# Performance work log

Measured on AMD Instinct MI355X. Metric: run time of the kernel, lower is better.

## Reference

```python
import jax, jax.numpy as jnp
import numpy as np

N_NODES = 100000
N_GRAPHS = 512


def gcn_conv(x, W, b, src, dst, n):
    # PyG GCNConv: h = x @ W; add self-loops; sym-normalize; scatter-add to dst; + bias
    h = x @ W
    loop = jnp.arange(n, dtype=src.dtype)
    s = jnp.concatenate([src, loop])
    d = jnp.concatenate([dst, loop])
    deg = jax.ops.segment_sum(jnp.ones_like(d, dtype=h.dtype), d, num_segments=n)
    dinv = jnp.where(deg > 0, jax.lax.rsqrt(deg), 0.0)
    norm = dinv[s] * dinv[d]               # [E+N]
    msg = h[s] * norm[:, None]             # gather + scale
    out = jax.ops.segment_sum(msg, d, num_segments=n)
    return out + b


def setup_inputs() -> dict:
    key = jax.random.key(0)
    ks = jax.random.split(key, 12)
    F_in, H, C = 128, 128, 10
    x = jax.random.normal(ks[0], (N_NODES, F_in), dtype=jnp.float32)
    edge_index = jax.random.randint(ks[1], (2, 3200000), 0, N_NODES, dtype=jnp.int64)
    batch = jnp.sort(jax.random.randint(ks[2], (N_NODES,), 0, N_GRAPHS, dtype=jnp.int64))
    def glorot(k, fi, fo):
        s = jnp.sqrt(6.0 / (fi + fo))
        return jax.random.uniform(k, (fi, fo), dtype=jnp.float32, minval=-s, maxval=s)
    return {
        "x": x, "edge_index": edge_index, "batch": batch,
        "W_in": glorot(ks[3], F_in, H), "b_in": jnp.zeros((H,), jnp.float32),
        "W_h0": glorot(ks[4], H, H), "b_h0": jnp.zeros((H,), jnp.float32),
        "W_h1": glorot(ks[5], H, H), "b_h1": jnp.zeros((H,), jnp.float32),
        "W_out": glorot(ks[6], H, C), "b_out": jnp.zeros((C,), jnp.float32),
    }


def reference(x, edge_index, batch, W_in, b_in, W_h0, b_h0, W_h1, b_h1, W_out, b_out):
    src, dst = edge_index[0], edge_index[1]
    n = x.shape[0]
    h = jax.nn.relu(gcn_conv(x, W_in, b_in, src, dst, n))
    h = jax.nn.relu(gcn_conv(h, W_h0, b_h0, src, dst, n))
    h = jax.nn.relu(gcn_conv(h, W_h1, b_h1, src, dst, n))
    h = gcn_conv(h, W_out, b_out, src, dst, n)
    # global_mean_pool over graph ids
    sums = jax.ops.segment_sum(h, batch, num_segments=N_GRAPHS)
    cnts = jax.ops.segment_sum(jnp.ones((n,), h.dtype), batch, num_segments=N_GRAPHS)
    pooled = sums / jnp.maximum(cnts, 1.0)[:, None]
    return jax.nn.log_softmax(pooled, axis=-1)
```

## Files before the change

kernel.cpp:

```cpp
#include <hip/hip_runtime.h>
#include <math.h>

#define TPB 256
#define MAXDEG 80
#define SHIFT 8
#define BNODES 256
#define CAP 10240
#define EPB 4096
#define LSTR 136

typedef short bf16x8 __attribute__((ext_vector_type(8)));
typedef float f32x4 __attribute__((ext_vector_type(4)));

__device__ inline unsigned short f2bf(float f) {
    unsigned u = __float_as_uint(f);
    return (unsigned short)((u + 0x7fffu + ((u >> 16) & 1u)) >> 16);
}
__device__ inline float bflo(unsigned u) { return __uint_as_float(u << 16); }
__device__ inline float bfhi(unsigned u) { return __uint_as_float(u & 0xffff0000u); }



__global__ __launch_bounds__(TPB) void p1_k(const int* __restrict__ src,
                                            const int* __restrict__ dst,
                                            int* __restrict__ gbcnt,
                                            int* __restrict__ buckets, int E, int nb) {
    __shared__ int hist[512];
    __shared__ int lcur[512];
    int tid = threadIdx.x;
    for (int b = tid; b < nb; b += TPB) hist[b] = 0;
    __syncthreads();
    int e0 = blockIdx.x * EPB;
    int m = E - e0; if (m > EPB) m = EPB;
    for (int i = tid; i < m; i += TPB)
        atomicAdd(&hist[dst[e0 + i] >> SHIFT], 1);
    __syncthreads();
    for (int b = tid; b < nb; b += TPB) {
        int h = hist[b];
        lcur[b] = h ? atomicAdd(&gbcnt[b], h) : 0;
    }
    __syncthreads();
    for (int i = tid; i < m; i += TPB) {
        int d = dst[e0 + i];
        int s = src[e0 + i];
        int b = d >> SHIFT;
        int pos = atomicAdd(&lcur[b], 1);
        if (pos < CAP) buckets[(size_t)b * CAP + pos] = (s << SHIFT) | (d & (BNODES - 1));
    }
}


__global__ __launch_bounds__(TPB) void p2_k(const int* __restrict__ gbcnt,
                                            const int* __restrict__ buckets,
                                            int* __restrict__ csr,
                                            int* __restrict__ deg,
                                            float* __restrict__ dinv, int n, int nb,
                                            const float* __restrict__ W0,
                                            const float* __restrict__ W1,
                                            const float* __restrict__ W2,
                                            const float* __restrict__ W3,
                                            unsigned short* __restrict__ T0,
                                            unsigned short* __restrict__ T1,
                                            unsigned short* __restrict__ T2,
                                            unsigned short* __restrict__ T3,
                                            float* __restrict__ pool,
                                            int* __restrict__ cnt, int ng) {
    int b = blockIdx.x, tid = threadIdx.x;
    if (b >= nb) {
        int widx = b - nb;
        if (widx < 3) {
            const float* W = widx == 0 ? W0 : (widx == 1 ? W1 : W2);
            unsigned short* T = widx == 0 ? T0 : (widx == 1 ? T1 : T2);
            for (int idx = tid; idx < 16384; idx += TPB) {
                int nn = idx >> 7, kk = idx & 127;
                T[idx] = f2bf(W[kk * 128 + nn]);
            }
        } else {
            for (int idx = tid; idx < 2048; idx += TPB) {
                int nn = idx >> 7, kk = idx & 127;
                T3[idx] = nn < 10 ? f2bf(W3[kk * 10 + nn]) : (unsigned short)0;
            }
            for (int i = tid; i < ng * 10; i += TPB) pool[i] = 0.f;
            for (int i = tid; i < ng; i += TPB) cnt[i] = 0;
        }
        return;
    }
    __shared__ int lcnt[BNODES];
    lcnt[tid] = 0;
    __syncthreads();
    int m = gbcnt[b]; if (m > CAP) m = CAP;
    const int* bp = buckets + (size_t)b * CAP;
    int vb = b << SHIFT;
    for (int i = tid; i < m; i += TPB) {
        int rec = bp[i];
        int dl = rec & (BNODES - 1);
        int pos = atomicAdd(&lcnt[dl], 1);
        if (pos < MAXDEG) csr[(size_t)(vb + dl) * MAXDEG + pos] = rec >> SHIFT;
    }
    __syncthreads();
    int v = vb + tid;
    if (v < n) {
        int c = lcnt[tid];
        deg[v] = c < MAXDEG ? c : MAXDEG;
        dinv[v] = rsqrtf((float)(c + 1));
    }
}


__device__ __forceinline__ void mfma_tile(const unsigned short* Hs,
                                          const unsigned short* __restrict__ WT,
                                          const float* __restrict__ dinv,
                                          unsigned short* __restrict__ gout,
                                          int vb, int n, int w, int l) {
    f32x4 acc[2][8];
#pragma unroll
    for (int a = 0; a < 2; a++)
#pragma unroll
        for (int b = 0; b < 8; b++)
#pragma unroll
            for (int j = 0; j < 4; j++) acc[a][b][j] = 0.f;
    const int quad = l >> 4, lm = l & 15;
    const int mrow0 = w * 32;
#pragma unroll
    for (int ks = 0; ks < 4; ks++) {
        bf16x8 a0 = *(const bf16x8*)(Hs + (mrow0 + lm) * LSTR + ks * 32 + quad * 8);
        bf16x8 a1 = *(const bf16x8*)(Hs + (mrow0 + 16 + lm) * LSTR + ks * 32 + quad * 8);
#pragma unroll
        for (int nt = 0; nt < 8; nt++) {
            bf16x8 bf = *(const bf16x8*)(WT + (size_t)(nt * 16 + lm) * 128 + ks * 32 + quad * 8);
            acc[0][nt] = __builtin_amdgcn_mfma_f32_16x16x32_bf16(a0, bf, acc[0][nt], 0, 0, 0);
            acc[1][nt] = __builtin_amdgcn_mfma_f32_16x16x32_bf16(a1, bf, acc[1][nt], 0, 0, 0);
        }
    }
#pragma unroll
    for (int mt = 0; mt < 2; mt++) {
#pragma unroll
        for (int j = 0; j < 4; j++) {
            int r = vb + mrow0 + mt * 16 + quad * 4 + j;
            if (r < n) {
                float s = dinv[r];
#pragma unroll
                for (int nt = 0; nt < 8; nt++) {
                    size_t base = ((size_t)((nt >> 1) * n + r)) * 32;
                    gout[base + (nt & 1) * 16 + lm] = f2bf(acc[mt][nt][j] * s);
                }
            }
        }
    }
}


__global__ __launch_bounds__(256) void gemm_f32in(const float* __restrict__ x,
                                                  const unsigned short* __restrict__ WT,
                                                  const float* __restrict__ dinv,
                                                  unsigned short* __restrict__ gout, int n) {
    __shared__ unsigned short Hs[128 * LSTR];
    int tid = threadIdx.x;
    int vb = blockIdx.x * 128;
    for (int i = tid; i < 8192; i += 256) {
        int row = i >> 6, cw = i & 63;
        int gr = vb + row; if (gr > n - 1) gr = n - 1;
        float2 xv = *(const float2*)(x + (size_t)gr * 128 + cw * 2);
        unsigned pk = ((unsigned)f2bf(xv.y) << 16) | f2bf(xv.x);
        *(unsigned*)(Hs + row * LSTR + cw * 2) = pk;
    }
    __syncthreads();
    mfma_tile(Hs, WT, dinv, gout, vb, n, tid >> 6, tid & 63);
}


__global__ __launch_bounds__(256) void gemm_bf16in(const unsigned* __restrict__ hin,
                                                   const unsigned short* __restrict__ WT,
                                                   const float* __restrict__ dinv,
                                                   unsigned short* __restrict__ gout, int n) {
    __shared__ unsigned short Hs[128 * LSTR];
    int tid = threadIdx.x;
    int vb = blockIdx.x * 128;
    for (int i = tid; i < 8192; i += 256) {
        int row = i >> 6, cw = i & 63;
        int gr = vb + row; if (gr > n - 1) gr = n - 1;
        *(unsigned*)(Hs + row * LSTR + cw * 2) =
            hin[((size_t)((cw >> 4) * n + gr)) * 16 + (cw & 15)];
    }
    __syncthreads();
    mfma_tile(Hs, WT, dinv, gout, vb, n, tid >> 6, tid & 63);
}


__global__ __launch_bounds__(256) void thin_mfma(const unsigned* __restrict__ hin,
                                                 const unsigned short* __restrict__ WT3,
                                                 const float* __restrict__ dinv,
                                                 unsigned* __restrict__ g4u, int n) {
    __shared__ unsigned short Hs[128 * LSTR];
    int tid = threadIdx.x;
    int vb = blockIdx.x * 128;
    for (int i = tid; i < 8192; i += 256) {
        int row = i >> 6, cw = i & 63;
        int gr = vb + row; if (gr > n - 1) gr = n - 1;
        *(unsigned*)(Hs + row * LSTR + cw * 2) =
            hin[((size_t)((cw >> 4) * n + gr)) * 16 + (cw & 15)];
    }
    __syncthreads();
    int w = tid >> 6, l = tid & 63;
    int quad = l >> 4, lm = l & 15;
    int mrow0 = w * 32;
    f32x4 acc[2];
#pragma unroll
    for (int a = 0; a < 2; a++)
#pragma unroll
        for (int j = 0; j < 4; j++) acc[a][j] = 0.f;
#pragma unroll
    for (int ks = 0; ks < 4; ks++) {
        bf16x8 a0 = *(const bf16x8*)(Hs + (mrow0 + lm) * LSTR + ks * 32 + quad * 8);
        bf16x8 a1 = *(const bf16x8*)(Hs + (mrow0 + 16 + lm) * LSTR + ks * 32 + quad * 8);
        bf16x8 bf = *(const bf16x8*)(WT3 + (size_t)lm * 128 + ks * 32 + quad * 8);
        acc[0] = __builtin_amdgcn_mfma_f32_16x16x32_bf16(a0, bf, acc[0], 0, 0, 0);
        acc[1] = __builtin_amdgcn_mfma_f32_16x16x32_bf16(a1, bf, acc[1], 0, 0, 0);
    }
#pragma unroll
    for (int mt = 0; mt < 2; mt++) {
#pragma unroll
        for (int j = 0; j < 4; j++) {
            float self = acc[mt][j];
            float part = __shfl_down(self, 1, 64);
            int r = vb + mrow0 + mt * 16 + quad * 4 + j;
            if ((lm & 1) == 0 && lm < 10 && r < n) {
                float s = dinv[r];
                g4u[(size_t)r * 5 + (lm >> 1)] =
                    ((unsigned)f2bf(part * s) << 16) | f2bf(self * s);
            }
        }
    }
}


__global__ __launch_bounds__(256) void aggq_k(const unsigned* __restrict__ G,
                                              const float* __restrict__ dinv,
                                              const int* __restrict__ deg,
                                              const int* __restrict__ csr,
                                              const float* __restrict__ bias,
                                              unsigned* __restrict__ H, int n, int nblk) {
    int q = blockIdx.x / nblk;
    int blk = blockIdx.x - q * nblk;
    int w = threadIdx.x >> 6, l = threadIdx.x & 63;
    int sub = l >> 4, t = l & 15;
    int v = blk * 16 + w * 4 + sub;
    if (v >= n) return;
    const unsigned* Gq = G + (size_t)q * n * 16;
    unsigned u = Gq[(size_t)v * 16 + t];
    float a0 = bflo(u), a1 = bfhi(u);
    const int* cp = csr + (size_t)v * MAXDEG;
    int d = deg[v];
    int e = 0;
    for (; e + 8 <= d; e += 8) {
        int s0 = cp[e], s1 = cp[e + 1], s2 = cp[e + 2], s3 = cp[e + 3];
        int s4 = cp[e + 4], s5 = cp[e + 5], s6 = cp[e + 6], s7 = cp[e + 7];
        unsigned u0 = Gq[(size_t)s0 * 16 + t];
        unsigned u1 = Gq[(size_t)s1 * 16 + t];
        unsigned u2 = Gq[(size_t)s2 * 16 + t];
        unsigned u3 = Gq[(size_t)s3 * 16 + t];
        unsigned u4 = Gq[(size_t)s4 * 16 + t];
        unsigned u5 = Gq[(size_t)s5 * 16 + t];
        unsigned u6 = Gq[(size_t)s6 * 16 + t];
        unsigned u7 = Gq[(size_t)s7 * 16 + t];
        a0 += (bflo(u0) + bflo(u1)) + (bflo(u2) + bflo(u3))
            + (bflo(u4) + bflo(u5)) + (bflo(u6) + bflo(u7));
        a1 += (bfhi(u0) + bfhi(u1)) + (bfhi(u2) + bfhi(u3))
            + (bfhi(u4) + bfhi(u5)) + (bfhi(u6) + bfhi(u7));
    }
    for (; e < d; e++) {
        unsigned ux = Gq[(size_t)cp[e] * 16 + t];
        a0 += bflo(ux); a1 += bfhi(ux);
    }
    float2 bb = *(const float2*)(bias + q * 32 + 2 * t);
    float s = dinv[v];
    float o0 = fmaxf(s * a0 + bb.x, 0.f);
    float o1 = fmaxf(s * a1 + bb.y, 0.f);
    H[((size_t)q * n + v) * 16 + t] = ((unsigned)f2bf(o1) << 16) | f2bf(o0);
}


__global__ __launch_bounds__(TPB) void agg_thin_bf(const unsigned* __restrict__ g4u,
                                                   const float* __restrict__ dinv,
                                                   const int* __restrict__ deg,
                                                   const int* __restrict__ csr,
                                                   const float* __restrict__ bias,
                                                   float* __restrict__ out, int n) {
    int idx = blockIdx.x * TPB + threadIdx.x;
    if (idx >= n * 5) return;
    int v = idx / 5, t = idx - v * 5;
    unsigned u = g4u[(size_t)v * 5 + t];
    float acc0 = bflo(u), acc1 = bfhi(u);
    const int* cp = csr + (size_t)v * MAXDEG;
    int d = deg[v];
    int e = 0;
    for (; e + 4 <= d; e += 4) {
        unsigned u0 = g4u[(size_t)cp[e] * 5 + t];
        unsigned u1 = g4u[(size_t)cp[e + 1] * 5 + t];
        unsigned u2 = g4u[(size_t)cp[e + 2] * 5 + t];
        unsigned u3 = g4u[(size_t)cp[e + 3] * 5 + t];
        acc0 += (bflo(u0) + bflo(u1)) + (bflo(u2) + bflo(u3));
        acc1 += (bfhi(u0) + bfhi(u1)) + (bfhi(u2) + bfhi(u3));
    }
    for (; e < d; e++) {
        unsigned ux = g4u[(size_t)cp[e] * 5 + t];
        acc0 += bflo(ux); acc1 += bfhi(ux);
    }
    float s = dinv[v];
    out[(size_t)v * 10 + 2 * t]     = s * acc0 + bias[2 * t];
    out[(size_t)v * 10 + 2 * t + 1] = s * acc1 + bias[2 * t + 1];
}


#define POOL_SPAN 8

__global__ __launch_bounds__(TPB) void pool_k(const float* __restrict__ h,
                                              const int* __restrict__ batch,
                                              float* __restrict__ pool, int* __restrict__ cnt, int n) {
    __shared__ float lp[POOL_SPAN][10];
    __shared__ int lc[POOL_SPAN];
    __shared__ int g0;
    int tid = threadIdx.x;
    int v = blockIdx.x * TPB + tid;
    if (tid == 0) {
        int first = blockIdx.x * TPB;
        if (first > n - 1) first = n - 1;
        g0 = batch[first];
    }
    if (tid < POOL_SPAN) lc[tid] = 0;
    if (tid < POOL_SPAN * 10) lp[tid / 10][tid % 10] = 0.f;
    __syncthreads();
    if (v < n) {
        int gi = batch[v];
        int o = gi - g0;
        if (o < POOL_SPAN) {
            atomicAdd(&lc[o], 1);
#pragma unroll
            for (int c = 0; c < 10; c++) atomicAdd(&lp[o][c], h[(size_t)v * 10 + c]);
        } else {
            atomicAdd(&cnt[gi], 1);
#pragma unroll
            for (int c = 0; c < 10; c++) atomicAdd(&pool[gi * 10 + c], h[(size_t)v * 10 + c]);
        }
    }
    __syncthreads();
    if (tid < POOL_SPAN) {
        if (lc[tid] > 0) atomicAdd(&cnt[g0 + tid], lc[tid]);
    }
    if (tid < POOL_SPAN * 10) {
        int o = tid / 10, c = tid % 10;
        if (lc[o] > 0) atomicAdd(&pool[(g0 + o) * 10 + c], lp[o][c]);
    }
}

__global__ __launch_bounds__(TPB) void final_k(const float* __restrict__ pool,
                                               const int* __restrict__ cnt,
                                               float* __restrict__ out, int ng) {
    int gi = blockIdx.x * TPB + threadIdx.x;
    if (gi >= ng) return;
    float cn = fmaxf((float)cnt[gi], 1.f);
    float x[10];
    float m = -1e30f;
#pragma unroll
    for (int c = 0; c < 10; c++) {
        x[c] = pool[gi * 10 + c] / cn;
        m = fmaxf(m, x[c]);
    }
    float s = 0.f;
#pragma unroll
    for (int c = 0; c < 10; c++) s += expf(x[c] - m);
    float l = logf(s);
#pragma unroll
    for (int c = 0; c < 10; c++) out[gi * 10 + c] = x[c] - m - l;
}


extern "C" void kernel_launch(void* const* d_in, const int* in_sizes, int n_in,
                              void* d_out, int out_size, void* d_ws, size_t ws_size,
                              hipStream_t stream) {
    const float* x    = (const float*)d_in[0];
    const int*   ei   = (const int*)d_in[1];
    const int*   batch= (const int*)d_in[2];
    const float* W_in = (const float*)d_in[3];
    const float* b_in = (const float*)d_in[4];
    const float* W_h0 = (const float*)d_in[5];
    const float* b_h0 = (const float*)d_in[6];
    const float* W_h1 = (const float*)d_in[7];
    const float* b_h1 = (const float*)d_in[8];
    const float* W_out= (const float*)d_in[9];
    const float* b_out= (const float*)d_in[10];

    const int n  = in_sizes[2];
    const int E  = in_sizes[1] / 2;
    const int ng = out_size / 10;
    const int nb = (n + BNODES - 1) >> SHIFT;

    char* p = (char*)d_ws;
    auto carve = [&](size_t bytes) { void* r = (void*)p; p += (bytes + 255) & ~(size_t)255; return r; };
    int*            deg    = (int*)           carve((size_t)n * 4);
    float*          dinv   = (float*)         carve((size_t)n * 4);
    int*            gbcnt  = (int*)           carve((size_t)nb * 4);
    int*            buckets= (int*)           carve((size_t)nb * CAP * 4);
    int*            csr    = (int*)           carve((size_t)n * MAXDEG * 4);
    unsigned*       G      = (unsigned*)      carve((size_t)n * 64 * 4);
    unsigned*       H      = (unsigned*)      carve((size_t)n * 64 * 4);
    unsigned short* WT0    = (unsigned short*)carve(16384 * 2);
    unsigned short* WT1    = (unsigned short*)carve(16384 * 2);
    unsigned short* WT2    = (unsigned short*)carve(16384 * 2);
    unsigned short* WT3    = (unsigned short*)carve(2048 * 2);
    unsigned*       g4u    = (unsigned*)      carve((size_t)n * 5 * 4);
    float*          h10    = (float*)         carve((size_t)n * 10 * 4);
    float*          pool   = (float*)         carve((size_t)ng * 10 * 4);
    int*            cnt    = (int*)           carve((size_t)ng * 4);

    (void)hipMemsetAsync(gbcnt, 0, (size_t)nb * 4, stream);

    const int gN = (n + TPB - 1) / TPB;
    const int gP1 = (E + EPB - 1) / EPB;
    const int gG = (n + 127) / 128;
    const int nblk = (n + 15) / 16;
    const int gAq = 4 * nblk;

    p1_k<<<gP1, TPB, 0, stream>>>(ei, ei + E, gbcnt, buckets, E, nb);
    p2_k<<<nb + 4, TPB, 0, stream>>>(gbcnt, buckets, csr, deg, dinv, n, nb,
                                     W_in, W_h0, W_h1, W_out, WT0, WT1, WT2, WT3,
                                     pool, cnt, ng);

    gemm_f32in<<<gG, 256, 0, stream>>>(x, WT0, dinv, (unsigned short*)G, n);
    aggq_k<<<gAq, 256, 0, stream>>>(G, dinv, deg, csr, b_in, H, n, nblk);
    gemm_bf16in<<<gG, 256, 0, stream>>>(H, WT1, dinv, (unsigned short*)G, n);
    aggq_k<<<gAq, 256, 0, stream>>>(G, dinv, deg, csr, b_h0, H, n, nblk);
    gemm_bf16in<<<gG, 256, 0, stream>>>(H, WT2, dinv, (unsigned short*)G, n);
    aggq_k<<<gAq, 256, 0, stream>>>(G, dinv, deg, csr, b_h1, H, n, nblk);
    thin_mfma<<<gG, 256, 0, stream>>>(H, WT3, dinv, g4u, n);
    agg_thin_bf<<<(n * 5 + TPB - 1) / TPB, TPB, 0, stream>>>(g4u, dinv, deg, csr, b_out, h10, n);
    pool_k<<<gN, TPB, 0, stream>>>(h10, batch, pool, cnt, n);
    final_k<<<(ng + TPB - 1) / TPB, TPB, 0, stream>>>(pool, cnt, (float*)d_out, ng);
}
```

Baseline: 762.1 us.

## Split hidden features into two column halves instead of four quarters

```diff
diff --git a/kernel.cpp b/kernel.cpp
--- a/kernel.cpp
+++ b/kernel.cpp
@@ -141,8 +141,8 @@
                 float s = dinv[r];
 #pragma unroll
                 for (int nt = 0; nt < 8; nt++) {
-                    size_t base = ((size_t)((nt >> 1) * n + r)) * 32;
-                    gout[base + (nt & 1) * 16 + lm] = f2bf(acc[mt][nt][j] * s);
+                    gout[((size_t)((nt >> 2) * n + r)) * 64 + (nt & 3) * 16 + lm] =
+                        f2bf(acc[mt][nt][j] * s);
                 }
             }
         }
@@ -180,7 +180,7 @@
         int row = i >> 6, cw = i & 63;
         int gr = vb + row; if (gr > n - 1) gr = n - 1;
         *(unsigned*)(Hs + row * LSTR + cw * 2) =
-            hin[((size_t)((cw >> 4) * n + gr)) * 16 + (cw & 15)];
+            hin[((size_t)((cw >> 5) * n + gr)) * 32 + (cw & 31)];
     }
     __syncthreads();
     mfma_tile(Hs, WT, dinv, gout, vb, n, tid >> 6, tid & 63);
@@ -198,7 +198,7 @@
         int row = i >> 6, cw = i & 63;
         int gr = vb + row; if (gr > n - 1) gr = n - 1;
         *(unsigned*)(Hs + row * LSTR + cw * 2) =
-            hin[((size_t)((cw >> 4) * n + gr)) * 16 + (cw & 15)];
+            hin[((size_t)((cw >> 5) * n + gr)) * 32 + (cw & 31)];
     }
     __syncthreads();
     int w = tid >> 6, l = tid & 63;
@@ -234,20 +234,20 @@
 }
 
 
-__global__ __launch_bounds__(256) void aggq_k(const unsigned* __restrict__ G,
+__global__ __launch_bounds__(256) void aggh_k(const unsigned* __restrict__ G,
                                               const float* __restrict__ dinv,
                                               const int* __restrict__ deg,
                                               const int* __restrict__ csr,
                                               const float* __restrict__ bias,
                                               unsigned* __restrict__ H, int n, int nblk) {
-    int q = blockIdx.x / nblk;
-    int blk = blockIdx.x - q * nblk;
+    int hh = blockIdx.x / nblk;
+    int blk = blockIdx.x - hh * nblk;
     int w = threadIdx.x >> 6, l = threadIdx.x & 63;
-    int sub = l >> 4, t = l & 15;
-    int v = blk * 16 + w * 4 + sub;
+    int sub = l >> 5, t = l & 31;
+    int v = blk * 8 + w * 2 + sub;
     if (v >= n) return;
-    const unsigned* Gq = G + (size_t)q * n * 16;
-    unsigned u = Gq[(size_t)v * 16 + t];
+    const unsigned* Gh = G + (size_t)hh * n * 32;
+    unsigned u = Gh[(size_t)v * 32 + t];
     float a0 = bflo(u), a1 = bfhi(u);
     const int* cp = csr + (size_t)v * MAXDEG;
     int d = deg[v];
@@ -255,28 +255,28 @@
     for (; e + 8 <= d; e += 8) {
         int s0 = cp[e], s1 = cp[e + 1], s2 = cp[e + 2], s3 = cp[e + 3];
         int s4 = cp[e + 4], s5 = cp[e + 5], s6 = cp[e + 6], s7 = cp[e + 7];
-        unsigned u0 = Gq[(size_t)s0 * 16 + t];
-        unsigned u1 = Gq[(size_t)s1 * 16 + t];
-        unsigned u2 = Gq[(size_t)s2 * 16 + t];
-        unsigned u3 = Gq[(size_t)s3 * 16 + t];
-        unsigned u4 = Gq[(size_t)s4 * 16 + t];
-        unsigned u5 = Gq[(size_t)s5 * 16 + t];
-        unsigned u6 = Gq[(size_t)s6 * 16 + t];
-        unsigned u7 = Gq[(size_t)s7 * 16 + t];
+        unsigned u0 = Gh[(size_t)s0 * 32 + t];
+        unsigned u1 = Gh[(size_t)s1 * 32 + t];
+        unsigned u2 = Gh[(size_t)s2 * 32 + t];
+        unsigned u3 = Gh[(size_t)s3 * 32 + t];
+        unsigned u4 = Gh[(size_t)s4 * 32 + t];
+        unsigned u5 = Gh[(size_t)s5 * 32 + t];
+        unsigned u6 = Gh[(size_t)s6 * 32 + t];
+        unsigned u7 = Gh[(size_t)s7 * 32 + t];
         a0 += (bflo(u0) + bflo(u1)) + (bflo(u2) + bflo(u3))
             + (bflo(u4) + bflo(u5)) + (bflo(u6) + bflo(u7));
         a1 += (bfhi(u0) + bfhi(u1)) + (bfhi(u2) + bfhi(u3))
             + (bfhi(u4) + bfhi(u5)) + (bfhi(u6) + bfhi(u7));
     }
     for (; e < d; e++) {
-        unsigned ux = Gq[(size_t)cp[e] * 16 + t];
+        unsigned ux = Gh[(size_t)cp[e] * 32 + t];
         a0 += bflo(ux); a1 += bfhi(ux);
     }
-    float2 bb = *(const float2*)(bias + q * 32 + 2 * t);
+    float2 bb = *(const float2*)(bias + hh * 64 + 2 * t);
     float s = dinv[v];
     float o0 = fmaxf(s * a0 + bb.x, 0.f);
     float o1 = fmaxf(s * a1 + bb.y, 0.f);
-    H[((size_t)q * n + v) * 16 + t] = ((unsigned)f2bf(o1) << 16) | f2bf(o0);
+    H[((size_t)hh * n + v) * 32 + t] = ((unsigned)f2bf(o1) << 16) | f2bf(o0);
 }
 
 
@@ -418,8 +418,8 @@
     const int gN = (n + TPB - 1) / TPB;
     const int gP1 = (E + EPB - 1) / EPB;
     const int gG = (n + 127) / 128;
-    const int nblk = (n + 15) / 16;
-    const int gAq = 4 * nblk;
+    const int nblk = (n + 7) / 8;
+    const int gAh = 2 * nblk;
 
     p1_k<<<gP1, TPB, 0, stream>>>(ei, ei + E, gbcnt, buckets, E, nb);
     p2_k<<<nb + 4, TPB, 0, stream>>>(gbcnt, buckets, csr, deg, dinv, n, nb,
@@ -427,11 +427,11 @@
                                      pool, cnt, ng);
 
     gemm_f32in<<<gG, 256, 0, stream>>>(x, WT0, dinv, (unsigned short*)G, n);
-    aggq_k<<<gAq, 256, 0, stream>>>(G, dinv, deg, csr, b_in, H, n, nblk);
+    aggh_k<<<gAh, 256, 0, stream>>>(G, dinv, deg, csr, b_in, H, n, nblk);
     gemm_bf16in<<<gG, 256, 0, stream>>>(H, WT1, dinv, (unsigned short*)G, n);
-    aggq_k<<<gAq, 256, 0, stream>>>(G, dinv, deg, csr, b_h0, H, n, nblk);
+    aggh_k<<<gAh, 256, 0, stream>>>(G, dinv, deg, csr, b_h0, H, n, nblk);
     gemm_bf16in<<<gG, 256, 0, stream>>>(H, WT2, dinv, (unsigned short*)G, n);
-    aggq_k<<<gAq, 256, 0, stream>>>(G, dinv, deg, csr, b_h1, H, n, nblk);
+    aggh_k<<<gAh, 256, 0, stream>>>(G, dinv, deg, csr, b_h1, H, n, nblk);
     thin_mfma<<<gG, 256, 0, stream>>>(H, WT3, dinv, g4u, n);
     agg_thin_bf<<<(n * 5 + TPB - 1) / TPB, TPB, 0, stream>>>(g4u, dinv, deg, csr, b_out, h10, n);
     pool_k<<<gN, TPB, 0, stream>>>(h10, batch, pool, cnt, n);
```

New measurement: 686.0 us. 1.11x faster.
